# Kernel optimization log

Hardware: AMD Instinct MI355X
Metric: run time of the kernel (lower is better)

## Reference

```python
import jax, jax.numpy as jnp
import numpy as np

D_K = 64  # per-head dim used for the 1/sqrt(d_k) scaling


def setup_inputs() -> dict:
    key = jax.random.key(0)
    k1, k2, k3, k4 = jax.random.split(key, 4)
    B, H, Lq, NB, NT, D = 4, 8, 512, 32, 128, 64
    q = jax.random.normal(k1, (B, H, Lq, D), dtype=jnp.float32)
    k = jax.random.normal(k2, (B, NB, H, NT, D), dtype=jnp.float32)
    v = jax.random.normal(k3, (B, NB, H, NT, D), dtype=jnp.float32)
    attn_s = jax.random.uniform(k4, (B, H, Lq, NB), dtype=jnp.float32)
    return {"q": q, "k": k, "v": v, "attn_s": attn_s}


def reference(q, k, v, attn_s):
    # q: [B,H,Lq,D]; k,v: [B,NB,H,NT,D]; attn_s: [B,H,Lq,NB]
    B, NB, H, NT, D = k.shape
    Lq = q.shape[2]
    scale = 1.0 / jnp.sqrt(jnp.asarray(D_K, dtype=q.dtype))
    # block-wise QK scores: [B,NB,H,Lq,NT] (q broadcast over blocks instead of expand+matmul)
    attn = jnp.einsum('bhqd,bnhtd->bnhqt', q * scale, k)
    weights = jax.nn.softmax(attn, axis=-1)            # per-block softmax over tokens
    attn_w = jnp.transpose(weights, (0, 2, 3, 1, 4))    # [B,H,Lq,NB,NT]
    attn_w = attn_w * attn_s[..., None]                 # sentence-level reweighting
    attn_w = attn_w.reshape(B, H, Lq, NB * NT)          # concat blocks (dropout p=0 -> identity)
    v_w = jnp.transpose(v, (0, 2, 1, 3, 4)).reshape(B, H, NB * NT, D)
    out = jnp.matmul(attn_w, v_w)                       # [B,H,Lq,D]
    out = jnp.transpose(out, (0, 2, 1, 3)).reshape(B, Lq, H * D)
    return out, attn_w
```

## Files before the change

### kernel.cpp

```cpp
#include <hip/hip_runtime.h>
#include <stdint.h>

constexpr int CB=4, CH=8, CLQ=512, CNB=32, CNT=128, CD=64;
constexpr int QT=16;
constexpr int PSTR=36;
constexpr int OSTR=68;

typedef __attribute__((ext_vector_type(8))) __fp16 half8;
typedef __attribute__((ext_vector_type(2))) __fp16 half2v;
typedef __attribute__((ext_vector_type(4))) float f32x4;

union HFrag { uint32_t u[4]; half8 h8; half2v h2[4]; };

__global__ __launch_bounds__(256, 4)
void sdpa_mfma_kernel(const float* __restrict__ qg, const float* __restrict__ kg,
                      const float* __restrict__ vg, const float* __restrict__ sg,
                      float* __restrict__ outg, float* __restrict__ awg)
{
    __shared__ __align__(16) float pbuf[4 * QT * PSTR];
    __shared__ __align__(16) float sums[2][64];
    __shared__ __align__(16) float as_t[CNB * QT];
    __shared__ __align__(16) float obuf[4 * QT * OSTR];

    const int tid  = threadIdx.x;
    const int wave = tid >> 6;
    const int lane = tid & 63;
    const int l15  = lane & 15;
    const int q8   = lane >> 4;

    const int bid = blockIdx.x;
    const int qt  = bid & 31;
    const int bh  = bid >> 5;
    const int b   = bh >> 3;
    const int h   = bh & 7;
    const int q0  = qt * QT;

    {
        const float* sbase = sg + ((size_t)bh * CLQ + q0) * CNB;
        #pragma unroll
        for (int e = 0; e < 2; ++e) {
            int idx = tid + e * 256;
            int r = idx >> 5, n = idx & 31;
            as_t[n * QT + r] = sbase[r * CNB + n];
        }
    }

    HFrag qf[2];
    {
        const float* qrow = qg + ((size_t)bh * CLQ + q0 + l15) * CD;
        #pragma unroll
        for (int s = 0; s < 2; ++s) {
            f32x4 a = *(const f32x4*)&qrow[s*32 + q8*8];
            f32x4 c = *(const f32x4*)&qrow[s*32 + q8*8 + 4];
            qf[s].h2[0] = __builtin_amdgcn_cvt_pkrtz(a[0]*0.125f, a[1]*0.125f);
            qf[s].h2[1] = __builtin_amdgcn_cvt_pkrtz(a[2]*0.125f, a[3]*0.125f);
            qf[s].h2[2] = __builtin_amdgcn_cvt_pkrtz(c[0]*0.125f, c[1]*0.125f);
            qf[s].h2[3] = __builtin_amdgcn_cvt_pkrtz(c[2]*0.125f, c[3]*0.125f);
        }
    }

    f32x4 O[4];
    #pragma unroll
    for (int cd = 0; cd < 4; ++cd) O[cd] = (f32x4){0.f,0.f,0.f,0.f};

    float* pw = &pbuf[wave * QT * PSTR];

    for (int n = 0; n < CNB; ++n) {
        const float* kb = kg + ((size_t)((b*CNB + n)*CH + h)) * CNT * CD;
        const float* vb = vg + ((size_t)((b*CNB + n)*CH + h)) * CNT * CD + wave*32*CD;

        f32x4 S[2];
        #pragma unroll
        for (int c = 0; c < 2; ++c) {
            const float* kr = kb + (size_t)(wave*32 + c*16 + l15) * CD;
            HFrag kf[2];
            #pragma unroll
            for (int s = 0; s < 2; ++s) {
                f32x4 a = *(const f32x4*)&kr[s*32 + q8*8];
                f32x4 d = *(const f32x4*)&kr[s*32 + q8*8 + 4];
                kf[s].h2[0] = __builtin_amdgcn_cvt_pkrtz(a[0], a[1]);
                kf[s].h2[1] = __builtin_amdgcn_cvt_pkrtz(a[2], a[3]);
                kf[s].h2[2] = __builtin_amdgcn_cvt_pkrtz(d[0], d[1]);
                kf[s].h2[3] = __builtin_amdgcn_cvt_pkrtz(d[2], d[3]);
            }
            f32x4 acc = (f32x4){0.f,0.f,0.f,0.f};
            acc = __builtin_amdgcn_mfma_f32_16x16x32_f16(qf[0].h8, kf[0].h8, acc, 0, 0, 0);
            acc = __builtin_amdgcn_mfma_f32_16x16x32_f16(qf[1].h8, kf[1].h8, acc, 0, 0, 0);
            S[c] = acc;
        }

        float E0[4], E1[4], ps[4];
        #pragma unroll
        for (int r = 0; r < 4; ++r) {
            E0[r] = __expf(S[0][r]);
            E1[r] = __expf(S[1][r]);
            ps[r] = E0[r] + E1[r];
        }
        #pragma unroll
        for (int off = 1; off <= 8; off <<= 1) {
            #pragma unroll
            for (int r = 0; r < 4; ++r) ps[r] += __shfl_xor(ps[r], off, 64);
        }
        if (l15 == 0) {
            f32x4 t = {ps[0], ps[1], ps[2], ps[3]};
            *(f32x4*)&sums[n & 1][wave*16 + q8*4] = t;
        }
        __syncthreads();

        f32x4 d4 = (f32x4){0.f,0.f,0.f,0.f};
        #pragma unroll
        for (int wv = 0; wv < 4; ++wv)
            d4 += *(const f32x4*)&sums[n & 1][wv*16 + q8*4];
        const f32x4 asv = *(const f32x4*)&as_t[n*QT + q8*4];

        float fac[4];
        #pragma unroll
        for (int r = 0; r < 4; ++r) fac[r] = asv[r] * __builtin_amdgcn_rcpf(d4[r]);

        #pragma unroll
        for (int r = 0; r < 4; ++r) {
            pw[(q8*4 + r)*PSTR + l15]      = E0[r] * fac[r];
            pw[(q8*4 + r)*PSTR + 16 + l15] = E1[r] * fac[r];
        }

        #pragma unroll
        for (int i = 0; i < 2; ++i) {
            int idx = lane + i*64;
            int row = idx >> 3, c4 = idx & 7;
            f32x4 pv = *(const f32x4*)&pw[row*PSTR + c4*4];
            *(f32x4*)&awg[(((size_t)bh*CLQ + q0 + row)*CNB + n)*CNT + wave*32 + c4*4] = pv;
        }

        HFrag pa;
        {
            f32x4 a = *(const f32x4*)&pw[l15*PSTR + q8*8];
            f32x4 c = *(const f32x4*)&pw[l15*PSTR + q8*8 + 4];
            pa.h2[0] = __builtin_amdgcn_cvt_pkrtz(a[0], a[1]);
            pa.h2[1] = __builtin_amdgcn_cvt_pkrtz(a[2], a[3]);
            pa.h2[2] = __builtin_amdgcn_cvt_pkrtz(c[0], c[1]);
            pa.h2[3] = __builtin_amdgcn_cvt_pkrtz(c[2], c[3]);
        }

        #pragma unroll
        for (int cd = 0; cd < 4; ++cd) {
            float vf[8];
            #pragma unroll
            for (int j = 0; j < 8; ++j)
                vf[j] = vb[(q8*8 + j)*CD + cd*16 + l15];
            HFrag vh;
            #pragma unroll
            for (int p = 0; p < 4; ++p)
                vh.h2[p] = __builtin_amdgcn_cvt_pkrtz(vf[2*p], vf[2*p+1]);
            O[cd] = __builtin_amdgcn_mfma_f32_16x16x32_f16(pa.h8, vh.h8, O[cd], 0, 0, 0);
        }
    }

    {
        float* ow = &obuf[wave * QT * OSTR];
        #pragma unroll
        for (int cd = 0; cd < 4; ++cd)
            #pragma unroll
            for (int r = 0; r < 4; ++r)
                ow[(q8*4 + r)*OSTR + cd*16 + l15] = O[cd][r];
    }
    __syncthreads();
    {
        int r = tid >> 4, dq = tid & 15;
        f32x4 acc = (f32x4){0.f,0.f,0.f,0.f};
        #pragma unroll
        for (int wv = 0; wv < 4; ++wv)
            acc += *(const f32x4*)&obuf[wv*QT*OSTR + r*OSTR + dq*4];
        *(f32x4*)&outg[((size_t)b*CLQ + q0 + r)*(CH*CD) + h*CD + dq*4] = acc;
    }
}

extern "C" void kernel_launch(void* const* d_in, const int* in_sizes, int n_in,
                              void* d_out, int out_size, void* d_ws, size_t ws_size,
                              hipStream_t stream) {
    const float* q = (const float*)d_in[0];
    const float* k = (const float*)d_in[1];
    const float* v = (const float*)d_in[2];
    const float* s = (const float*)d_in[3];
    float* out = (float*)d_out;
    float* aw  = out + (size_t)CB * CLQ * CH * CD;

    const int grid = CB * CH * (CLQ / QT);
    sdpa_mfma_kernel<<<grid, 256, 0, stream>>>(q, k, v, s, out, aw);
}
```

Before: 492.3 us.

## Split each block's work across eight waves with double-buffered probability tiles

Raises the block size from 4 to 8 waves. Each wave now computes scores for 16 tokens instead of 32, and each pair of waves shares a 32-token slice of the PV product, each wave covering half of the D columns. The probability tile is double-buffered by block parity so that only one barrier per block iteration is needed. Normalization is now applied when the tile is read back, not when it is written. This is meant to raise parallelism and hide the latency of the global K/V loads, at the cost of more shared-memory traffic, extra summation over 8 partial sums, and higher occupancy demands.

Result: slower. 516.7 us (+5.0%).

```diff
diff --git a/kernel.cpp b/kernel.cpp
--- a/kernel.cpp
+++ b/kernel.cpp
@@ -3,8 +3,10 @@
 
 constexpr int CB=4, CH=8, CLQ=512, CNB=32, CNT=128, CD=64;
 constexpr int QT=16;
-constexpr int PSTR=36;
+constexpr int PSTR=20;
 constexpr int OSTR=68;
+constexpr int TILE=QT*PSTR;
+constexpr int PBUF=8*TILE;
 
 typedef __attribute__((ext_vector_type(8))) __fp16 half8;
 typedef __attribute__((ext_vector_type(2))) __fp16 half2v;
@@ -12,15 +14,15 @@
 
 union HFrag { uint32_t u[4]; half8 h8; half2v h2[4]; };
 
-__global__ __launch_bounds__(256, 4)
+__global__ __launch_bounds__(512, 8)
 void sdpa_mfma_kernel(const float* __restrict__ qg, const float* __restrict__ kg,
                       const float* __restrict__ vg, const float* __restrict__ sg,
                       float* __restrict__ outg, float* __restrict__ awg)
 {
-    __shared__ __align__(16) float pbuf[4 * QT * PSTR];
-    __shared__ __align__(16) float sums[2][64];
-    __shared__ __align__(16) float as_t[CNB * QT];
-    __shared__ __align__(16) float obuf[4 * QT * OSTR];
+    __shared__ __align__(16) float smem[8704];
+    float* const pbuf = smem;
+    float* const sums = smem + 2*PBUF;
+    float* const as_t = smem + 2*PBUF + 256;
 
     const int tid  = threadIdx.x;
     const int wave = tid >> 6;
@@ -35,14 +37,13 @@
     const int h   = bh & 7;
     const int q0  = qt * QT;
 
+    const int grp = wave >> 1;
+    const int cdb = (wave & 1) * 2;
+
     {
         const float* sbase = sg + ((size_t)bh * CLQ + q0) * CNB;
-        #pragma unroll
-        for (int e = 0; e < 2; ++e) {
-            int idx = tid + e * 256;
-            int r = idx >> 5, n = idx & 31;
-            as_t[n * QT + r] = sbase[r * CNB + n];
-        }
+        int r = tid >> 5, n = tid & 31;
+        as_t[n * QT + r] = sbase[r * CNB + n];
     }
 
     HFrag qf[2];
@@ -59,20 +60,17 @@
         }
     }
 
-    f32x4 O[4];
-    #pragma unroll
-    for (int cd = 0; cd < 4; ++cd) O[cd] = (f32x4){0.f,0.f,0.f,0.f};
-
-    float* pw = &pbuf[wave * QT * PSTR];
+    f32x4 O[2];
+    O[0] = (f32x4){0.f,0.f,0.f,0.f};
+    O[1] = (f32x4){0.f,0.f,0.f,0.f};
 
     for (int n = 0; n < CNB; ++n) {
         const float* kb = kg + ((size_t)((b*CNB + n)*CH + h)) * CNT * CD;
-        const float* vb = vg + ((size_t)((b*CNB + n)*CH + h)) * CNT * CD + wave*32*CD;
+        const float* vb = vg + ((size_t)((b*CNB + n)*CH + h)) * CNT * CD;
 
-        f32x4 S[2];
-        #pragma unroll
-        for (int c = 0; c < 2; ++c) {
-            const float* kr = kb + (size_t)(wave*32 + c*16 + l15) * CD;
+        f32x4 acc = (f32x4){0.f,0.f,0.f,0.f};
+        {
+            const float* kr = kb + (size_t)(wave*16 + l15) * CD;
             HFrag kf[2];
             #pragma unroll
             for (int s = 0; s < 2; ++s) {
@@ -83,18 +81,15 @@
                 kf[s].h2[2] = __builtin_amdgcn_cvt_pkrtz(d[0], d[1]);
                 kf[s].h2[3] = __builtin_amdgcn_cvt_pkrtz(d[2], d[3]);
             }
-            f32x4 acc = (f32x4){0.f,0.f,0.f,0.f};
             acc = __builtin_amdgcn_mfma_f32_16x16x32_f16(qf[0].h8, kf[0].h8, acc, 0, 0, 0);
             acc = __builtin_amdgcn_mfma_f32_16x16x32_f16(qf[1].h8, kf[1].h8, acc, 0, 0, 0);
-            S[c] = acc;
         }
 
-        float E0[4], E1[4], ps[4];
+        float E[4], ps[4];
         #pragma unroll
         for (int r = 0; r < 4; ++r) {
-            E0[r] = __expf(S[0][r]);
-            E1[r] = __expf(S[1][r]);
-            ps[r] = E0[r] + E1[r];
+            E[r]  = __expf(acc[r]);
+            ps[r] = E[r];
         }
         #pragma unroll
         for (int off = 1; off <= 8; off <<= 1) {
@@ -103,74 +98,80 @@
         }
         if (l15 == 0) {
             f32x4 t = {ps[0], ps[1], ps[2], ps[3]};
-            *(f32x4*)&sums[n & 1][wave*16 + q8*4] = t;
+            *(f32x4*)&sums[(n & 1)*128 + wave*QT + q8*4] = t;
         }
+
+        float* pw = pbuf + (n & 1)*PBUF + wave*TILE;
+        #pragma unroll
+        for (int r = 0; r < 4; ++r)
+            pw[(q8*4 + r)*PSTR + l15] = E[r];
+
         __syncthreads();
 
-        f32x4 d4 = (f32x4){0.f,0.f,0.f,0.f};
-        #pragma unroll
-        for (int wv = 0; wv < 4; ++wv)
-            d4 += *(const f32x4*)&sums[n & 1][wv*16 + q8*4];
-        const f32x4 asv = *(const f32x4*)&as_t[n*QT + q8*4];
+        const float* sb = &sums[(n & 1)*128];
 
-        float fac[4];
-        #pragma unroll
-        for (int r = 0; r < 4; ++r) fac[r] = asv[r] * __builtin_amdgcn_rcpf(d4[r]);
-
-        #pragma unroll
-        for (int r = 0; r < 4; ++r) {
-            pw[(q8*4 + r)*PSTR + l15]      = E0[r] * fac[r];
-            pw[(q8*4 + r)*PSTR + 16 + l15] = E1[r] * fac[r];
-        }
-
-        #pragma unroll
-        for (int i = 0; i < 2; ++i) {
-            int idx = lane + i*64;
-            int row = idx >> 3, c4 = idx & 7;
+        {
+            int row = lane >> 2, c4 = lane & 3;
+            float d = 0.f;
+            #pragma unroll
+            for (int w = 0; w < 8; ++w) d += sb[w*QT + row];
+            float fr = as_t[n*QT + row] * __builtin_amdgcn_rcpf(d);
             f32x4 pv = *(const f32x4*)&pw[row*PSTR + c4*4];
-            *(f32x4*)&awg[(((size_t)bh*CLQ + q0 + row)*CNB + n)*CNT + wave*32 + c4*4] = pv;
+            pv[0] *= fr; pv[1] *= fr; pv[2] *= fr; pv[3] *= fr;
+            *(f32x4*)&awg[(((size_t)bh*CLQ + q0 + row)*CNB + n)*CNT + wave*16 + c4*4] = pv;
         }
 
         HFrag pa;
         {
-            f32x4 a = *(const f32x4*)&pw[l15*PSTR + q8*8];
-            f32x4 c = *(const f32x4*)&pw[l15*PSTR + q8*8 + 4];
-            pa.h2[0] = __builtin_amdgcn_cvt_pkrtz(a[0], a[1]);
-            pa.h2[1] = __builtin_amdgcn_cvt_pkrtz(a[2], a[3]);
-            pa.h2[2] = __builtin_amdgcn_cvt_pkrtz(c[0], c[1]);
-            pa.h2[3] = __builtin_amdgcn_cvt_pkrtz(c[2], c[3]);
+            float dA = 0.f;
+            #pragma unroll
+            for (int w = 0; w < 8; ++w) dA += sb[w*QT + l15];
+            float fA = as_t[n*QT + l15] * __builtin_amdgcn_rcpf(dA);
+            const float* pt = pbuf + (n & 1)*PBUF + ((wave & ~1) + (q8 >> 1))*TILE
+                              + l15*PSTR + (q8 & 1)*8;
+            f32x4 a = *(const f32x4*)&pt[0];
+            f32x4 c = *(const f32x4*)&pt[4];
+            pa.h2[0] = __builtin_amdgcn_cvt_pkrtz(a[0]*fA, a[1]*fA);
+            pa.h2[1] = __builtin_amdgcn_cvt_pkrtz(a[2]*fA, a[3]*fA);
+            pa.h2[2] = __builtin_amdgcn_cvt_pkrtz(c[0]*fA, c[1]*fA);
+            pa.h2[3] = __builtin_amdgcn_cvt_pkrtz(c[2]*fA, c[3]*fA);
         }
 
-        #pragma unroll
-        for (int cd = 0; cd < 4; ++cd) {
-            float vf[8];
+        {
+            const float* vrow = vb + (size_t)(grp*32 + q8*8)*CD + l15;
             #pragma unroll
-            for (int j = 0; j < 8; ++j)
-                vf[j] = vb[(q8*8 + j)*CD + cd*16 + l15];
-            HFrag vh;
-            #pragma unroll
-            for (int p = 0; p < 4; ++p)
-                vh.h2[p] = __builtin_amdgcn_cvt_pkrtz(vf[2*p], vf[2*p+1]);
-            O[cd] = __builtin_amdgcn_mfma_f32_16x16x32_f16(pa.h8, vh.h8, O[cd], 0, 0, 0);
+            for (int c = 0; c < 2; ++c) {
+                float vf[8];
+                #pragma unroll
+                for (int j = 0; j < 8; ++j)
+                    vf[j] = vrow[j*CD + (cdb + c)*16];
+                HFrag vh;
+                #pragma unroll
+                for (int p = 0; p < 4; ++p)
+                    vh.h2[p] = __builtin_amdgcn_cvt_pkrtz(vf[2*p], vf[2*p+1]);
+                O[c] = __builtin_amdgcn_mfma_f32_16x16x32_f16(pa.h8, vh.h8, O[c], 0, 0, 0);
+            }
         }
     }
 
+    __syncthreads();
     {
-        float* ow = &obuf[wave * QT * OSTR];
+        float* ow = smem + wave * QT * OSTR;
         #pragma unroll
-        for (int cd = 0; cd < 4; ++cd)
+        for (int c = 0; c < 2; ++c)
             #pragma unroll
             for (int r = 0; r < 4; ++r)
-                ow[(q8*4 + r)*OSTR + cd*16 + l15] = O[cd][r];
+                ow[(q8*4 + r)*OSTR + (cdb + c)*16 + l15] = O[c][r];
     }
     __syncthreads();
-    {
+    if (tid < 256) {
         int r = tid >> 4, dq = tid & 15;
-        f32x4 acc = (f32x4){0.f,0.f,0.f,0.f};
+        int sel = (dq >> 3) & 1;
+        f32x4 acc2 = (f32x4){0.f,0.f,0.f,0.f};
         #pragma unroll
-        for (int wv = 0; wv < 4; ++wv)
-            acc += *(const f32x4*)&obuf[wv*QT*OSTR + r*OSTR + dq*4];
-        *(f32x4*)&outg[((size_t)b*CLQ + q0 + r)*(CH*CD) + h*CD + dq*4] = acc;
+        for (int g = 0; g < 4; ++g)
+            acc2 += *(const f32x4*)&smem[(2*g + sel)*QT*OSTR + r*OSTR + dq*4];
+        *(f32x4*)&outg[((size_t)b*CLQ + q0 + r)*(CH*CD) + h*CD + dq*4] = acc2;
     }
 }
 
@@ -185,5 +186,5 @@
     float* aw  = out + (size_t)CB * CLQ * CH * CD;
 
     const int grid = CB * CH * (CLQ / QT);
-    sdpa_mfma_kernel<<<grid, 256, 0, stream>>>(q, k, v, s, out, aw);
+    sdpa_mfma_kernel<<<grid, 512, 0, stream>>>(q, k, v, s, out, aw);
 }
```

## Prefetch next block's K/V into registers and defer softmax normalization past PV MFMA

Applied to the files above, without the earlier changes.

Loads K and V for the next block into registers while the current block is computed, a software-pipelining step meant to hide global memory latency. The per-block barrier is moved after the PV MFMA: unnormalized exponentials feed the MFMA, and the result is scaled by attn_s/sum afterwards. This takes the cross-wave sum reduction off the critical path before the matrix multiply. The cost is many more registers per thread (kraw plus vraw), which can reduce occupancy under the 256x4 launch bounds. The fp16 input to the PV MFMA is now unnormalized exp values, which changes rounding slightly.

Result: slower. 513.0 us (+4.2%).

```diff
diff --git a/kernel.cpp b/kernel.cpp
--- a/kernel.cpp
+++ b/kernel.cpp
@@ -5,6 +5,7 @@
 constexpr int QT=16;
 constexpr int PSTR=36;
 constexpr int OSTR=68;
+constexpr int NSTRIDE=CH*CNT*CD;
 
 typedef __attribute__((ext_vector_type(8))) __fp16 half8;
 typedef __attribute__((ext_vector_type(2))) __fp16 half2v;
@@ -59,25 +60,41 @@
         }
     }
 
+    const float* kcur = kg + ((size_t)(b*CNB)*CH + h) * CNT * CD + (size_t)(wave*32 + l15) * CD;
+    const float* vcur = vg + ((size_t)(b*CNB)*CH + h) * CNT * CD + (size_t)(wave*32 + q8*8) * CD + l15;
+
+    f32x4 kraw[8];
+    float vraw[32];
+    #pragma unroll
+    for (int c = 0; c < 2; ++c)
+        #pragma unroll
+        for (int s = 0; s < 2; ++s) {
+            kraw[c*4 + s*2 + 0] = *(const f32x4*)&kcur[c*16*CD + s*32 + q8*8];
+            kraw[c*4 + s*2 + 1] = *(const f32x4*)&kcur[c*16*CD + s*32 + q8*8 + 4];
+        }
+    #pragma unroll
+    for (int cd = 0; cd < 4; ++cd)
+        #pragma unroll
+        for (int j = 0; j < 8; ++j)
+            vraw[cd*8 + j] = vcur[j*CD + cd*16];
+
     f32x4 O[4];
     #pragma unroll
     for (int cd = 0; cd < 4; ++cd) O[cd] = (f32x4){0.f,0.f,0.f,0.f};
 
     float* pw = &pbuf[wave * QT * PSTR];
 
+    __syncthreads();
+
     for (int n = 0; n < CNB; ++n) {
-        const float* kb = kg + ((size_t)((b*CNB + n)*CH + h)) * CNT * CD;
-        const float* vb = vg + ((size_t)((b*CNB + n)*CH + h)) * CNT * CD + wave*32*CD;
-
         f32x4 S[2];
         #pragma unroll
         for (int c = 0; c < 2; ++c) {
-            const float* kr = kb + (size_t)(wave*32 + c*16 + l15) * CD;
             HFrag kf[2];
             #pragma unroll
             for (int s = 0; s < 2; ++s) {
-                f32x4 a = *(const f32x4*)&kr[s*32 + q8*8];
-                f32x4 d = *(const f32x4*)&kr[s*32 + q8*8 + 4];
+                f32x4 a = kraw[c*4 + s*2 + 0];
+                f32x4 d = kraw[c*4 + s*2 + 1];
                 kf[s].h2[0] = __builtin_amdgcn_cvt_pkrtz(a[0], a[1]);
                 kf[s].h2[1] = __builtin_amdgcn_cvt_pkrtz(a[2], a[3]);
                 kf[s].h2[2] = __builtin_amdgcn_cvt_pkrtz(d[0], d[1]);
@@ -89,6 +106,18 @@
             S[c] = acc;
         }
 
+        if (n + 1 < CNB) {
+            const float* kn = kcur + NSTRIDE;
+            #pragma unroll
+            for (int c = 0; c < 2; ++c)
+                #pragma unroll
+                for (int s = 0; s < 2; ++s) {
+                    kraw[c*4 + s*2 + 0] = *(const f32x4*)&kn[c*16*CD + s*32 + q8*8];
+                    kraw[c*4 + s*2 + 1] = *(const f32x4*)&kn[c*16*CD + s*32 + q8*8 + 4];
+                }
+            kcur = kn;
+        }
+
         float E0[4], E1[4], ps[4];
         #pragma unroll
         for (int r = 0; r < 4; ++r) {
@@ -105,30 +134,10 @@
             f32x4 t = {ps[0], ps[1], ps[2], ps[3]};
             *(f32x4*)&sums[n & 1][wave*16 + q8*4] = t;
         }
-        __syncthreads();
-
-        f32x4 d4 = (f32x4){0.f,0.f,0.f,0.f};
-        #pragma unroll
-        for (int wv = 0; wv < 4; ++wv)
-            d4 += *(const f32x4*)&sums[n & 1][wv*16 + q8*4];
-        const f32x4 asv = *(const f32x4*)&as_t[n*QT + q8*4];
-
-        float fac[4];
-        #pragma unroll
-        for (int r = 0; r < 4; ++r) fac[r] = asv[r] * __builtin_amdgcn_rcpf(d4[r]);
-
         #pragma unroll
         for (int r = 0; r < 4; ++r) {
-            pw[(q8*4 + r)*PSTR + l15]      = E0[r] * fac[r];
-            pw[(q8*4 + r)*PSTR + 16 + l15] = E1[r] * fac[r];
-        }
-
-        #pragma unroll
-        for (int i = 0; i < 2; ++i) {
-            int idx = lane + i*64;
-            int row = idx >> 3, c4 = idx & 7;
-            f32x4 pv = *(const f32x4*)&pw[row*PSTR + c4*4];
-            *(f32x4*)&awg[(((size_t)bh*CLQ + q0 + row)*CNB + n)*CNT + wave*32 + c4*4] = pv;
+            pw[(q8*4 + r)*PSTR + l15]      = E0[r];
+            pw[(q8*4 + r)*PSTR + 16 + l15] = E1[r];
         }
 
         HFrag pa;
@@ -141,20 +150,55 @@
             pa.h2[3] = __builtin_amdgcn_cvt_pkrtz(c[2], c[3]);
         }
 
+        f32x4 T[4];
         #pragma unroll
         for (int cd = 0; cd < 4; ++cd) {
-            float vf[8];
-            #pragma unroll
-            for (int j = 0; j < 8; ++j)
-                vf[j] = vb[(q8*8 + j)*CD + cd*16 + l15];
             HFrag vh;
             #pragma unroll
             for (int p = 0; p < 4; ++p)
-                vh.h2[p] = __builtin_amdgcn_cvt_pkrtz(vf[2*p], vf[2*p+1]);
-            O[cd] = __builtin_amdgcn_mfma_f32_16x16x32_f16(pa.h8, vh.h8, O[cd], 0, 0, 0);
-        }
-    }
-
+                vh.h2[p] = __builtin_amdgcn_cvt_pkrtz(vraw[cd*8 + 2*p], vraw[cd*8 + 2*p + 1]);
+            T[cd] = __builtin_amdgcn_mfma_f32_16x16x32_f16(
+                        pa.h8, vh.h8, (f32x4){0.f,0.f,0.f,0.f}, 0, 0, 0);
+        }
+        if (n + 1 < CNB) {
+            const float* vn = vcur + NSTRIDE;
+            #pragma unroll
+            for (int cd = 0; cd < 4; ++cd)
+                #pragma unroll
+                for (int j = 0; j < 8; ++j)
+                    vraw[cd*8 + j] = vn[j*CD + cd*16];
+            vcur = vn;
+        }
+
+        __syncthreads();
+
+        f32x4 d4 = (f32x4){0.f,0.f,0.f,0.f};
+        #pragma unroll
+        for (int wv = 0; wv < 4; ++wv)
+            d4 += *(const f32x4*)&sums[n & 1][wv*16 + q8*4];
+        const f32x4 asv = *(const f32x4*)&as_t[n*QT + q8*4];
+        #pragma unroll
+        for (int r = 0; r < 4; ++r) {
+            float fac = asv[r] * __builtin_amdgcn_rcpf(d4[r]);
+            #pragma unroll
+            for (int cd = 0; cd < 4; ++cd)
+                O[cd][r] += fac * T[cd][r];
+        }
+
+        #pragma unroll
+        for (int i = 0; i < 2; ++i) {
+            int idx = lane + i*64;
+            int row = idx >> 3, c4 = idx & 7;
+            float dr = sums[n & 1][row] + sums[n & 1][16 + row]
+                     + sums[n & 1][32 + row] + sums[n & 1][48 + row];
+            float fr = as_t[n*QT + row] * __builtin_amdgcn_rcpf(dr);
+            f32x4 pv = *(const f32x4*)&pw[row*PSTR + c4*4];
+            pv[0] *= fr; pv[1] *= fr; pv[2] *= fr; pv[3] *= fr;
+            *(f32x4*)&awg[(((size_t)bh*CLQ + q0 + row)*CNB + n)*CNT + wave*32 + c4*4] = pv;
+        }
+    }
+
+    __syncthreads();
     {
         float* ow = &obuf[wave * QT * OSTR];
         #pragma unroll
```
